# Optimization experiments

Hardware: AMD Instinct MI355X
Metric: run time of the kernel (lower is better)

Reference implementation:

```python
import jax, jax.numpy as jnp
import numpy as np

E = 8          # num_global_experts (experts['count_per_node'])
D = 1024       # model_dim
H = 2048       # expert hidden_size
TOP_K = 2      # gate_type['k']


def setup_inputs() -> dict:
    key = jax.random.key(0)
    k_x, k_g, k_w1, k_w2 = jax.random.split(key, 4)
    B, S = 4, 2048
    inp = {
        "input": jax.random.normal(k_x, (B, S, D), dtype=jnp.float32),
        "Wg": jax.random.normal(k_g, (D, E), dtype=jnp.float32) * 0.02,
        "W1": jax.random.normal(k_w1, (E, D, H), dtype=jnp.float32) * 0.02,
        "b1": jnp.zeros((E, H), dtype=jnp.float32),
        "W2": jax.random.normal(k_w2, (E, H, D), dtype=jnp.float32) * 0.02,
        "b2": jnp.zeros((E, D), dtype=jnp.float32),
    }
    return inp


def reference(input, Wg, W1, b1, W2, b2):
    # ---- router: top-k softmax gating, gate weights normalized over top-k ----
    logits = jnp.einsum("bsd,de->bse", input, Wg)            # [B,S,E]
    probs = jax.nn.softmax(logits, axis=-1)                   # [B,S,E]
    top_vals, top_idx = jax.lax.top_k(probs, TOP_K)           # [B,S,K]
    top_vals = top_vals / jnp.sum(top_vals, axis=-1, keepdims=True)
    onehot = jax.nn.one_hot(top_idx, E, dtype=input.dtype)    # [B,S,K,E]
    mask = jnp.sum(onehot, axis=2)                            # [B,S,E] 0/1 dispatch mask (indices)
    scores = jnp.sum(onehot * top_vals[..., None], axis=2)    # [B,S,E] combine weights

    # ---- dense masked dispatch: repeat input per expert, mask non-routed tokens ----
    xm = input[None] * jnp.moveaxis(mask, -1, 0)[..., None]   # [E,B,S,D]

    # ---- per-expert 2-layer MLP (LinearExperts) ----
    h = jnp.einsum("ebsd,edh->ebsh", xm, W1) + b1[:, None, None, :]
    h = jax.nn.relu(h)                                        # [E,B,S,H]
    y = jnp.einsum("ebsh,ehd->ebsd", h, W2) + b2[:, None, None, :]

    # ---- weighted combine: sum_e expert_out * gate score ----
    out = jnp.sum(y * jnp.moveaxis(scores, -1, 0)[..., None], axis=0)  # [B,S,D]
    return out
```

## Files before the change

### kernel.cpp

```cpp
#include <hip/hip_runtime.h>
#include <hip/hip_bf16.h>

typedef __bf16 bf16x8 __attribute__((ext_vector_type(8)));
typedef __bf16 bf16x4 __attribute__((ext_vector_type(4)));
typedef float  f32x4  __attribute__((ext_vector_type(4)));

#define T_TOK    8192
#define D_DIM    1024
#define H_DIM    2048
#define E_NUM    8
#define MAX_MB   136
#define MAX_ROWS 17408

#define OFF_MBTOT   512
#define OFF_MB2E    1024
#define OFF_MBROW0  2048
#define OFF_TOPKE   4096
#define OFF_TOPKS   69632
#define OFF_TOK     135168
#define OFF_ROWIDX  204800
#define OFF_XB      (1u<<20)
#define OFF_W1T     (18u*1024*1024)
#define OFF_W2T     (50u*1024*1024)
#define OFF_HBUF    (82u*1024*1024)
#define OFF_YBUF    OFF_XB

__device__ __forceinline__ void gload_lds16(const void* g, void* l) {
    __builtin_amdgcn_global_load_lds(
        (const __attribute__((address_space(1))) void*)g,
        (__attribute__((address_space(3))) void*)l, 16, 0, 0);
}

__global__ __launch_bounds__(256) void k_router_cvt(
    const float* __restrict__ x, const float* __restrict__ Wg,
    __bf16* __restrict__ xb, int* __restrict__ topk_e, float* __restrict__ topk_s)
{
    __shared__ float wgT[E_NUM][1032];
    const int tid = threadIdx.x;
#pragma unroll
    for (int i = 0; i < 32; ++i) {
        int f = tid + i * 256;
        wgT[f & 7][f >> 3] = Wg[f];
    }
    __syncthreads();

    const int wave = tid >> 6, lane = tid & 63;
    const int t = blockIdx.x * 4 + wave;
    const float* xr = x + (size_t)t * D_DIM;
    __bf16* xbr = xb + (size_t)t * D_DIM;

    float acc[E_NUM];
#pragma unroll
    for (int e = 0; e < E_NUM; ++e) acc[e] = 0.f;

#pragma unroll
    for (int j = 0; j < 4; ++j) {
        const int d0 = lane * 4 + j * 256;
        float4 xv = *(const float4*)(xr + d0);
        bf16x4 o = { (__bf16)xv.x, (__bf16)xv.y, (__bf16)xv.z, (__bf16)xv.w };
        *(bf16x4*)(xbr + d0) = o;
#pragma unroll
        for (int e = 0; e < E_NUM; ++e) {
            float4 wv = *(const float4*)&wgT[e][d0];
            acc[e] += xv.x * wv.x + xv.y * wv.y + xv.z * wv.z + xv.w * wv.w;
        }
    }
#pragma unroll
    for (int off = 32; off >= 1; off >>= 1)
#pragma unroll
        for (int e = 0; e < E_NUM; ++e) acc[e] += __shfl_xor(acc[e], off, 64);

    if (lane == 0) {
        int e0 = 0; float v0 = acc[0];
#pragma unroll
        for (int e = 1; e < E_NUM; ++e) if (acc[e] > v0) { v0 = acc[e]; e0 = e; }
        int e1 = -1; float v1 = -1e30f;
#pragma unroll
        for (int e = 0; e < E_NUM; ++e) if (e != e0 && acc[e] > v1) { v1 = acc[e]; e1 = e; }
        float s0 = 1.f / (1.f + __expf(v1 - v0));
        float s1 = 1.f - s0;
        topk_e[t*2+0] = e0; topk_e[t*2+1] = e1;
        topk_s[t*2+0] = s0; topk_s[t*2+1] = s1;
    }
}

#define SORT_T 256
__global__ __launch_bounds__(512) void k_sort(
    const int* __restrict__ topk_e,
    int* __restrict__ mbTot, int* __restrict__ mb2e, int* __restrict__ mbrow0,
    int* __restrict__ tok, int* __restrict__ rowidx)
{
    __shared__ int lcnt[E_NUM][SORT_T];
    __shared__ int base[E_NUM];
    __shared__ int etot[E_NUM];
    const int tid = threadIdx.x;

    if (tid < SORT_T) {
#pragma unroll
        for (int e = 0; e < E_NUM; ++e) lcnt[e][tid] = 0;
    }
    __syncthreads();

    if (tid < SORT_T) {
        const int4* p = (const int4*)(topk_e + tid * 64);
#pragma unroll
        for (int i = 0; i < 16; ++i) {
            int4 v = p[i];
            lcnt[v.x][tid]++; lcnt[v.y][tid]++; lcnt[v.z][tid]++; lcnt[v.w][tid]++;
        }
    }
    __syncthreads();

    {
        const int w = tid >> 6, l = tid & 63;
        int v0 = lcnt[w][l*4+0], v1 = lcnt[w][l*4+1], v2 = lcnt[w][l*4+2], v3 = lcnt[w][l*4+3];
        int s = v0 + v1 + v2 + v3;
        int inc = s;
#pragma unroll
        for (int off = 1; off < 64; off <<= 1) {
            int o = __shfl_up(inc, off, 64);
            if (l >= off) inc += o;
        }
        int exc = inc - s;
        lcnt[w][l*4+0] = exc;
        lcnt[w][l*4+1] = exc + v0;
        lcnt[w][l*4+2] = exc + v0 + v1;
        lcnt[w][l*4+3] = exc + v0 + v1 + v2;
        if (l == 63) etot[w] = inc;
    }
    __syncthreads();

    if (tid == 0) {
        int row = 0, mb = 0;
        for (int e = 0; e < E_NUM; ++e) {
            base[e] = row;
            int nb = (etot[e] + 127) >> 7;
            for (int b = 0; b < nb; ++b) { mb2e[mb] = e; mbrow0[mb] = row + b*128; ++mb; }
            row += nb * 128;
        }
        mbTot[0] = mb;
    }
    __syncthreads();

    if (tid < SORT_T) {
#pragma unroll
        for (int e = 0; e < E_NUM; ++e) lcnt[e][tid] += base[e];
        const int4* p = (const int4*)(topk_e + tid * 64);
#pragma unroll
        for (int i = 0; i < 16; ++i) {
            int4 v = p[i];
            int j0 = tid * 64 + i * 4;
            int r;
            r = lcnt[v.x][tid]++; tok[r] = (j0+0) >> 1; rowidx[j0+0] = r;
            r = lcnt[v.y][tid]++; tok[r] = (j0+1) >> 1; rowidx[j0+1] = r;
            r = lcnt[v.z][tid]++; tok[r] = (j0+2) >> 1; rowidx[j0+2] = r;
            r = lcnt[v.w][tid]++; tok[r] = (j0+3) >> 1; rowidx[j0+3] = r;
        }
    }
}

__global__ __launch_bounds__(256) void k_transpose(
    const float* __restrict__ in, __bf16* __restrict__ out, int R, int C)
{
    __shared__ float tile[64][65];
    const int e = blockIdx.z;
    const float* inp = in + (size_t)e * R * C;
    __bf16* outp = out + (size_t)e * R * C;
    const int r0 = blockIdx.x * 64, c0 = blockIdx.y * 64;
    const int c = threadIdx.x & 63, rr = threadIdx.x >> 6;
#pragma unroll
    for (int i = 0; i < 16; ++i) {
        int r = rr + i * 4;
        tile[r][c] = inp[(size_t)(r0 + r) * C + c0 + c];
    }
    __syncthreads();
#pragma unroll
    for (int i = 0; i < 16; ++i) {
        int cc = rr + i * 4;
        outp[(size_t)(c0 + cc) * R + r0 + c] = (__bf16)tile[c][cc];
    }
}


#define LDSB_OFF 24576

#define BARR __builtin_amdgcn_s_barrier()
#define WVM3 asm volatile("s_waitcnt vmcnt(3)" ::: "memory")
#define WVM0 asm volatile("s_waitcnt vmcnt(0)" ::: "memory")
#define P1 __builtin_amdgcn_s_setprio(1)
#define P0 __builtin_amdgcn_s_setprio(0)

#define STAGE(BS_, T_) { \
    gload_lds16(pA  + (T_)*32, smem + (BS_)*8192 + wq); \
    gload_lds16(pB0 + (T_)*32, smem + LDSB_OFF + (BS_)*16384 + wq); \
    gload_lds16(pB1 + (T_)*32, smem + LDSB_OFF + (BS_)*16384 + 8192 + wq); }

#define RD_TILE(BS_) { \
    const char* ba = smem + (BS_)*8192; \
    const char* bb = smem + LDSB_OFF + (BS_)*16384; \
    av[0] = *(const bf16x8*)(ba + (wm*64 +  0 + r)*64 + qx); \
    av[1] = *(const bf16x8*)(ba + (wm*64 + 16 + r)*64 + qx); \
    av[2] = *(const bf16x8*)(ba + (wm*64 + 32 + r)*64 + qx); \
    av[3] = *(const bf16x8*)(ba + (wm*64 + 48 + r)*64 + qx); \
    bv[0] = *(const bf16x8*)(bb + (wn*64 +  0 + r)*64 + qx); \
    bv[1] = *(const bf16x8*)(bb + (wn*64 + 16 + r)*64 + qx); \
    bv[2] = *(const bf16x8*)(bb + (wn*64 + 32 + r)*64 + qx); \
    bv[3] = *(const bf16x8*)(bb + (wn*64 + 48 + r)*64 + qx); }

#define MFMA16 { \
    _Pragma("unroll") \
    for (int mi = 0; mi < 4; ++mi) \
    _Pragma("unroll") \
    for (int ni = 0; ni < 4; ++ni) \
        acc[mi][ni] = __builtin_amdgcn_mfma_f32_16x16x32_bf16(av[mi], bv[ni], acc[mi][ni], 0, 0, 0); }

template<int KD, int NBLK, bool GATHER, bool RELU>
__global__ __launch_bounds__(512, 4) void k_gemm(
    const __bf16* __restrict__ Asrc, const __bf16* __restrict__ WT,
    const float* __restrict__ bias, const int* __restrict__ tok,
    const int* __restrict__ mb2e, const int* __restrict__ mbrow0,
    const int* __restrict__ mbTot, __bf16* __restrict__ outp)
{
    constexpr int NT = KD / 32;
    constexpr int NOUT = NBLK * 256;
    __shared__ __align__(16) char smem[73728];

    const int id   = blockIdx.x;
    const int xcd  = id & 7;
    const int j    = id >> 3;
    const int nblk = j % NBLK;
    const int mbi  = (j / NBLK) * 8 + xcd;
    if (mbi >= *mbTot) return;
    const int e    = mb2e[mbi];
    const int row0 = mbrow0[mbi];
    const int n0   = nblk * 256;

    const int tid = threadIdx.x;
    const int w = tid >> 6, l = tid & 63;
    const int r = l & 15, q = l >> 4;
    const int wm = w >> 2, wn = w & 3;
    const int wq = w * 1024;
    const int qx = (q ^ ((r >> 1) & 3)) * 16;

    const int cg = (tid & 3) ^ ((tid >> 3) & 3);
    const __bf16* Wb = WT + (size_t)e * ((size_t)NOUT * KD);
    const __bf16* pA;
    {
        int ar = row0 + (tid >> 2);
        pA = GATHER ? Asrc + (size_t)tok[ar] * KD + cg * 8
                    : Asrc + (size_t)ar * KD + cg * 8;
    }
    const __bf16* pB0 = Wb + (size_t)(n0 + (tid >> 2)) * KD + cg * 8;
    const __bf16* pB1 = Wb + (size_t)(n0 + 128 + (tid >> 2)) * KD + cg * 8;

    f32x4 acc[4][4];
#pragma unroll
    for (int mi = 0; mi < 4; ++mi)
#pragma unroll
        for (int ni = 0; ni < 4; ++ni) acc[mi][ni] = (f32x4){0.f, 0.f, 0.f, 0.f};

    bf16x8 av[4], bv[4];

    STAGE(0, 0); STAGE(1, 1);
    WVM3; BARR;

    int bs = 0, bs2 = 2;
    for (int t = 0; t < NT - 2; ++t) {
        RD_TILE(bs);
        STAGE(bs2, t + 2);
        P1; MFMA16; P0;
        WVM3;
        BARR;
        int nb = (bs == 2) ? 0 : bs + 1;
        bs2 = bs; bs = nb;
    }
    RD_TILE(bs);
    P1; MFMA16; P0;
    WVM0; BARR;
    bs = (bs == 2) ? 0 : bs + 1;
    RD_TILE(bs);
    P1; MFMA16; P0;

    const float* be = bias + (size_t)e * NOUT;
    float bb4[4];
#pragma unroll
    for (int ni = 0; ni < 4; ++ni) bb4[ni] = be[n0 + wn*64 + ni*16 + r];
#pragma unroll
    for (int mi = 0; mi < 4; ++mi)
#pragma unroll
        for (int reg = 0; reg < 4; ++reg) {
            int row = row0 + wm*64 + mi*16 + q*4 + reg;
            __bf16* orow = outp + (size_t)row * NOUT + n0 + wn*64;
#pragma unroll
            for (int ni = 0; ni < 4; ++ni) {
                float v = acc[mi][ni][reg] + bb4[ni];
                if (RELU) v = fmaxf(v, 0.f);
                orow[ni*16 + r] = (__bf16)v;
            }
        }
}

__global__ __launch_bounds__(256) void k_combine(
    const __bf16* __restrict__ ybuf, const int* __restrict__ rowidx,
    const float* __restrict__ topk_s, float* __restrict__ out)
{
    const int t = blockIdx.x;
    const int d0 = threadIdx.x * 4;
    const int r0 = rowidx[t*2+0], r1 = rowidx[t*2+1];
    const float s0 = topk_s[t*2+0], s1 = topk_s[t*2+1];
    bf16x4 y0 = *(const bf16x4*)(ybuf + (size_t)r0 * D_DIM + d0);
    bf16x4 y1 = *(const bf16x4*)(ybuf + (size_t)r1 * D_DIM + d0);
    float4 o;
    o.x = s0 * (float)y0[0] + s1 * (float)y1[0];
    o.y = s0 * (float)y0[1] + s1 * (float)y1[1];
    o.z = s0 * (float)y0[2] + s1 * (float)y1[2];
    o.w = s0 * (float)y0[3] + s1 * (float)y1[3];
    *(float4*)(out + (size_t)t * D_DIM + d0) = o;
}

extern "C" void kernel_launch(void* const* d_in, const int* in_sizes, int n_in,
                              void* d_out, int out_size, void* d_ws, size_t ws_size,
                              hipStream_t stream) {
    const float* x  = (const float*)d_in[0];
    const float* Wg = (const float*)d_in[1];
    const float* W1 = (const float*)d_in[2];
    const float* b1 = (const float*)d_in[3];
    const float* W2 = (const float*)d_in[4];
    const float* b2 = (const float*)d_in[5];
    float* out = (float*)d_out;
    char* ws = (char*)d_ws;

    int*   mbTot  = (int*)  (ws + OFF_MBTOT);
    int*   mb2e   = (int*)  (ws + OFF_MB2E);
    int*   mbrow0 = (int*)  (ws + OFF_MBROW0);
    int*   topk_e = (int*)  (ws + OFF_TOPKE);
    float* topk_s = (float*)(ws + OFF_TOPKS);
    int*   tok    = (int*)  (ws + OFF_TOK);
    int*   rowidx = (int*)  (ws + OFF_ROWIDX);
    __bf16* xb   = (__bf16*)(ws + OFF_XB);
    __bf16* W1T  = (__bf16*)(ws + OFF_W1T);
    __bf16* W2T  = (__bf16*)(ws + OFF_W2T);
    __bf16* hbuf = (__bf16*)(ws + OFF_HBUF);
    __bf16* ybuf = (__bf16*)(ws + OFF_YBUF);

    hipMemsetAsync(ws + OFF_TOK, 0, MAX_ROWS * sizeof(int), stream);

    k_router_cvt<<<T_TOK/4, 256, 0, stream>>>(x, Wg, xb, topk_e, topk_s);
    k_sort      <<<1, 512, 0, stream>>>(topk_e, mbTot, mb2e, mbrow0, tok, rowidx);
    k_transpose <<<dim3(D_DIM/64, H_DIM/64, E_NUM), 256, 0, stream>>>(W1, W1T, D_DIM, H_DIM);
    k_transpose <<<dim3(H_DIM/64, D_DIM/64, E_NUM), 256, 0, stream>>>(W2, W2T, H_DIM, D_DIM);

    k_gemm<D_DIM, 8, true,  true ><<<MAX_MB * 8, 512, 0, stream>>>(
        xb, W1T, b1, tok, mb2e, mbrow0, mbTot, hbuf);
    k_gemm<H_DIM, 4, false, false><<<MAX_MB * 4, 512, 0, stream>>>(
        hbuf, W2T, b2, tok, mb2e, mbrow0, mbTot, ybuf);

    k_combine<<<T_TOK, 256, 0, stream>>>(ybuf, rowidx, topk_s, out);
}
```

Measured before the change: 414.1 us.

## Deepen A-operand prefetch to four LDS slots, decoupling it from B staging

Splits the combined A/B tile staging so the gathered A (token) tile is prefetched three steps ahead in a 4-slot ring, while the B weight tile keeps its 3-slot ring two steps ahead. The aim is to hide the higher latency of the indirect token-gather loads behind more MFMA work. In exchange, LDS use per block grows from 72KB to 80KB, which may lower occupancy. The wait counts and the loop prologue and epilogue are reworked to match.

```diff
diff --git a/kernel.cpp b/kernel.cpp
--- a/kernel.cpp
+++ b/kernel.cpp
@@ -182,22 +182,24 @@
 }
 
 
-#define LDSB_OFF 24576
+#define LDSB_OFF 32768
 
 #define BARR __builtin_amdgcn_s_barrier()
+#define WVM4 asm volatile("s_waitcnt vmcnt(4)" ::: "memory")
 #define WVM3 asm volatile("s_waitcnt vmcnt(3)" ::: "memory")
 #define WVM0 asm volatile("s_waitcnt vmcnt(0)" ::: "memory")
 #define P1 __builtin_amdgcn_s_setprio(1)
 #define P0 __builtin_amdgcn_s_setprio(0)
 
-#define STAGE(BS_, T_) { \
-    gload_lds16(pA  + (T_)*32, smem + (BS_)*8192 + wq); \
-    gload_lds16(pB0 + (T_)*32, smem + LDSB_OFF + (BS_)*16384 + wq); \
-    gload_lds16(pB1 + (T_)*32, smem + LDSB_OFF + (BS_)*16384 + 8192 + wq); }
-
-#define RD_TILE(BS_) { \
-    const char* ba = smem + (BS_)*8192; \
-    const char* bb = smem + LDSB_OFF + (BS_)*16384; \
+#define STAGE_A(SL_, T_) { \
+    gload_lds16(pA + (T_)*32, smem + (SL_)*8192 + wq); }
+#define STAGE_B(SL_, T_) { \
+    gload_lds16(pB0 + (T_)*32, smem + LDSB_OFF + (SL_)*16384 + wq); \
+    gload_lds16(pB1 + (T_)*32, smem + LDSB_OFF + (SL_)*16384 + 8192 + wq); }
+
+#define RD_TILE(ASL_, BSL_) { \
+    const char* ba = smem + (ASL_)*8192; \
+    const char* bb = smem + LDSB_OFF + (BSL_)*16384; \
     av[0] = *(const bf16x8*)(ba + (wm*64 +  0 + r)*64 + qx); \
     av[1] = *(const bf16x8*)(ba + (wm*64 + 16 + r)*64 + qx); \
     av[2] = *(const bf16x8*)(ba + (wm*64 + 32 + r)*64 + qx); \
@@ -223,7 +225,7 @@
 {
     constexpr int NT = KD / 32;
     constexpr int NOUT = NBLK * 256;
-    __shared__ __align__(16) char smem[73728];
+    __shared__ __align__(16) char smem[81920];
 
     const int id   = blockIdx.x;
     const int xcd  = id & 7;
@@ -261,24 +263,35 @@
 
     bf16x8 av[4], bv[4];
 
-    STAGE(0, 0); STAGE(1, 1);
+    STAGE_B(0, 0); STAGE_A(0, 0);
+    STAGE_A(1, 1); STAGE_B(1, 1);
+    STAGE_A(2, 2);
+    WVM4; BARR;
+
+    int rb = 0;
+    for (int t = 0; t < NT - 3; ++t) {
+        RD_TILE(t & 3, rb);
+        int sb = (rb == 0) ? 2 : rb - 1;
+        STAGE_B(sb, t + 2);
+        STAGE_A((t + 3) & 3, t + 3);
+        P1; MFMA16; P0;
+        WVM4;
+        BARR;
+        rb = (rb == 2) ? 0 : rb + 1;
+    }
+    RD_TILE((NT - 3) & 3, rb);
+    {
+        int sb = (rb == 0) ? 2 : rb - 1;
+        STAGE_B(sb, NT - 1);
+    }
+    P1; MFMA16; P0;
     WVM3; BARR;
-
-    int bs = 0, bs2 = 2;
-    for (int t = 0; t < NT - 2; ++t) {
-        RD_TILE(bs);
-        STAGE(bs2, t + 2);
-        P1; MFMA16; P0;
-        WVM3;
-        BARR;
-        int nb = (bs == 2) ? 0 : bs + 1;
-        bs2 = bs; bs = nb;
-    }
-    RD_TILE(bs);
+    rb = (rb == 2) ? 0 : rb + 1;
+    RD_TILE((NT - 2) & 3, rb);
     P1; MFMA16; P0;
     WVM0; BARR;
-    bs = (bs == 2) ? 0 : bs + 1;
-    RD_TILE(bs);
+    rb = (rb == 2) ? 0 : rb + 1;
+    RD_TILE((NT - 1) & 3, rb);
     P1; MFMA16; P0;
 
     const float* be = bias + (size_t)e * NOUT;
```

New measurement: 416.9 us. About the same (+0.7%).
